# Performance work log

Measured on AMD Instinct MI355X. Metric: run time of the kernel, lower is better.

The kernel has to match this reference:

```python
import jax, jax.numpy as jnp
import numpy as np

BLOCK_SIZE = 128


def setup_inputs() -> dict:
    key = jax.random.key(0)
    kq, kk, kv = jax.random.split(key, 3)
    b, t, e = 16, 8192, 256
    Q = jax.random.normal(kq, (b, t, e), dtype=jnp.float32)
    K = jax.random.normal(kk, (b, t, e), dtype=jnp.float32)
    V = jax.random.normal(kv, (b, t, e), dtype=jnp.float32)
    return {"Q": Q, "K": K, "V": V}


def reference(Q, K, V):
    b, t, e = Q.shape
    bs = BLOCK_SIZE
    n = t // bs
    scale = 1.0 / jnp.sqrt(jnp.asarray(e, Q.dtype))
    Qb = Q.reshape(b, n, bs, e)
    Kb = K.reshape(b, n, bs, e)
    Vb = V.reshape(b, n, bs, e)
    # block-diagonal scores: [b, n, bs, bs]
    Z = jnp.einsum('bnqe,bnke->bnqk', Qb, Kb) * scale
    causal = jnp.triu(jnp.ones((bs, bs), dtype=bool), k=1)  # True above diagonal
    Z = jnp.where(causal, -jnp.inf, Z)
    A = jax.nn.softmax(Z, axis=-1)
    out = jnp.einsum('bnqk,bnke->bnqe', A, Vb).reshape(b, t, e)
    A_flat = A.reshape(b, t, bs)  # matches torch view(b, t, block_size)
    return out, A_flat
```

## Files before the change

kernel.cpp:

```cpp
#include <hip/hip_runtime.h>

#define T_  8192
#define E_  256
#define BS_ 128

typedef __attribute__((ext_vector_type(8))) short bf16x8;
typedef __attribute__((ext_vector_type(4))) float f32x4;

__device__ __forceinline__ unsigned short f2bf(float x) {
    unsigned int u = __float_as_uint(x);
    u += 0x7fffu + ((u >> 16) & 1u);
    return (unsigned short)(u >> 16);
}

__device__ __forceinline__ bf16x8 pack8(f32x4 a, f32x4 b) {
    bf16x8 r;
    r[0] = (short)f2bf(a[0]); r[1] = (short)f2bf(a[1]);
    r[2] = (short)f2bf(a[2]); r[3] = (short)f2bf(a[3]);
    r[4] = (short)f2bf(b[0]); r[5] = (short)f2bf(b[1]);
    r[6] = (short)f2bf(b[2]); r[7] = (short)f2bf(b[3]);
    return r;
}

__global__ __launch_bounds__(512, 4) void dba_fused(
        const float* __restrict__ Qg, const float* __restrict__ Kg,
        const float* __restrict__ Vg, float* __restrict__ Ag,
        float* __restrict__ Og)
{
    __shared__ unsigned short Sm[BS_ * E_];

    const int tid  = threadIdx.x;
    const int lane = tid & 63;
    const int w    = tid >> 6;
    const int cl   = lane & 15;
    const int g    = lane >> 4;
    const int bi   = blockIdx.x >> 6;
    const int ni   = blockIdx.x & 63;
    const int base  = (bi * T_ + ni * BS_) * E_;
    const int abase = (bi * T_ + ni * BS_) * BS_;

    {
        const int c4   = lane * 4;
        const int chnk = c4 >> 3;
        const int klow = c4 & 7;
        #pragma unroll 4
        for (int i = 0; i < 16; ++i) {
            const int n = i * 8 + w;
            f32x4 kv = __builtin_nontemporal_load((const f32x4*)(Kg + base + n * E_ + c4));
            const int cp = chnk ^ (n & 15);
            uint2 pk;
            pk.x = (unsigned)f2bf(kv[0]) | ((unsigned)f2bf(kv[1]) << 16);
            pk.y = (unsigned)f2bf(kv[2]) | ((unsigned)f2bf(kv[3]) << 16);
            *(uint2*)&Sm[n * E_ + cp * 8 + klow] = pk;
        }
    }
    __syncthreads();

    f32x4 acc[8];
    #pragma unroll
    for (int nt = 0; nt < 8; ++nt) acc[nt] = (f32x4){0.f, 0.f, 0.f, 0.f};

    const float* qp = Qg + base + (w * 16 + cl) * E_;
    f32x4 q0 = __builtin_nontemporal_load((const f32x4*)(qp + g * 8));
    f32x4 q1 = __builtin_nontemporal_load((const f32x4*)(qp + g * 8 + 4));

    for (int ks = 0; ks < 8; ++ks) {
        bf16x8 aq = pack8(q0, q1);
        if (ks < 7) {
            const int kn = (ks + 1) * 32 + g * 8;
            q0 = __builtin_nontemporal_load((const f32x4*)(qp + kn));
            q1 = __builtin_nontemporal_load((const f32x4*)(qp + kn + 4));
        }
        #pragma unroll
        for (int nt = 0; nt < 8; ++nt) {
            const int n  = nt * 16 + cl;
            const int cp = (ks * 4 + g) ^ cl;
            bf16x8 bk = *(const bf16x8*)&Sm[n * E_ + cp * 8];
            acc[nt] = __builtin_amdgcn_mfma_f32_16x16x32_bf16(aq, bk, acc[nt], 0, 0, 0);
        }
    }

    const float scale = 0.0625f;
    const float L2E   = 1.4426950408889634f;
    #pragma unroll
    for (int r = 0; r < 4; ++r) {
        const int q = w * 16 + g * 4 + r;
        float m = -__builtin_inff();
        #pragma unroll
        for (int nt = 0; nt < 8; ++nt) {
            const int c = nt * 16 + cl;
            float z = acc[nt][r] * scale;
            z = (c > q) ? -__builtin_inff() : z;
            acc[nt][r] = z;
            m = fmaxf(m, z);
        }
        m = fmaxf(m, __shfl_xor(m, 1));
        m = fmaxf(m, __shfl_xor(m, 2));
        m = fmaxf(m, __shfl_xor(m, 4));
        m = fmaxf(m, __shfl_xor(m, 8));
        float s = 0.f;
        #pragma unroll
        for (int nt = 0; nt < 8; ++nt) {
            const float p = exp2f((acc[nt][r] - m) * L2E);
            acc[nt][r] = p;
            s += p;
        }
        s += __shfl_xor(s, 1);
        s += __shfl_xor(s, 2);
        s += __shfl_xor(s, 4);
        s += __shfl_xor(s, 8);
        const float rinv = __builtin_amdgcn_rcpf(s);
        #pragma unroll
        for (int nt = 0; nt < 8; ++nt)
            acc[nt][r] *= rinv;
    }

    #pragma unroll
    for (int nt = 0; nt < 8; ++nt)
        #pragma unroll
        for (int r = 0; r < 4; ++r)
            Ag[abase + (w * 16 + g * 4 + r) * BS_ + nt * 16 + cl] = acc[nt][r];

    __syncthreads();

    {
        const int n  = tid & 255;
        const int kh = (tid >> 8) * 64;
        const int nx = n & 15;
        #pragma unroll 4
        for (int i = 0; i < 16; ++i) {
            const int k = kh + i * 4;
            const float* vp = Vg + base + k * E_ + n;
            const float v0 = __builtin_nontemporal_load(vp);
            const float v1 = __builtin_nontemporal_load(vp + E_);
            const float v2 = __builtin_nontemporal_load(vp + 2 * E_);
            const float v3 = __builtin_nontemporal_load(vp + 3 * E_);
            const int cp = (k >> 3) ^ nx;
            uint2 pk;
            pk.x = (unsigned)f2bf(v0) | ((unsigned)f2bf(v1) << 16);
            pk.y = (unsigned)f2bf(v2) | ((unsigned)f2bf(v3) << 16);
            *(uint2*)&Sm[n * BS_ + cp * 8 + (k & 7)] = pk;
        }
    }
    __syncthreads();

    f32x4 acc2[16];
    #pragma unroll
    for (int nt = 0; nt < 16; ++nt) acc2[nt] = (f32x4){0.f, 0.f, 0.f, 0.f};

    const float* ap = Ag + abase + (w * 16 + cl) * BS_;
    f32x4 a0 = *(const f32x4*)(ap + g * 8);
    f32x4 a1 = *(const f32x4*)(ap + g * 8 + 4);

    for (int ks = 0; ks < 4; ++ks) {
        bf16x8 fa = pack8(a0, a1);
        if (ks < 3) {
            const int kn = (ks + 1) * 32 + g * 8;
            a0 = *(const f32x4*)(ap + kn);
            a1 = *(const f32x4*)(ap + kn + 4);
        }
        #pragma unroll
        for (int nt = 0; nt < 16; ++nt) {
            const int nn = nt * 16 + cl;
            const int cp = (ks * 4 + g) ^ cl;
            bf16x8 bv = *(const bf16x8*)&Sm[nn * BS_ + cp * 8];
            acc2[nt] = __builtin_amdgcn_mfma_f32_16x16x32_bf16(fa, bv, acc2[nt], 0, 0, 0);
        }
    }

    #pragma unroll
    for (int nt = 0; nt < 16; ++nt)
        #pragma unroll
        for (int r = 0; r < 4; ++r)
            __builtin_nontemporal_store(acc2[nt][r],
                Og + base + (w * 16 + g * 4 + r) * E_ + nt * 16 + cl);
}

extern "C" void kernel_launch(void* const* d_in, const int* in_sizes, int n_in,
                              void* d_out, int out_size, void* d_ws, size_t ws_size,
                              hipStream_t stream) {
    const float* Q = (const float*)d_in[0];
    const float* K = (const float*)d_in[1];
    const float* V = (const float*)d_in[2];
    float* O = (float*)d_out;
    const int b = in_sizes[0] / (T_ * E_);
    float* A = O + (size_t)b * T_ * E_;
    dim3 grid(b * (T_ / BS_));
    dim3 block(512);
    dba_fused<<<grid, block, 0, stream>>>(Q, K, V, A, O);
}
```

Measured before the change: 438.7 us.

## Stage P in LDS and stream V from registers for the PV matmul

The PV stage is restructured. The softmax probabilities are written as bf16 into shared memory instead of being read back from global A. Each wave now owns 32 output columns and takes V directly from global into registers as the MFMA B operand, with V loads issued early and double-buffered across k-steps. This removes the global round-trip of A, the V staging pass through LDS and one barrier, and overlaps V loads with softmax. In exchange it raises register pressure (vb and acc2 arrays), and the scalar V loads are strided column-wise, which may coalesce less well.

```diff
diff --git a/kernel.cpp b/kernel.cpp
--- a/kernel.cpp
+++ b/kernel.cpp
@@ -20,6 +20,11 @@
     r[4] = (short)f2bf(b[0]); r[5] = (short)f2bf(b[1]);
     r[6] = (short)f2bf(b[2]); r[7] = (short)f2bf(b[3]);
     return r;
+}
+
+__device__ __forceinline__ void lds_barrier() {
+    asm volatile("s_waitcnt lgkmcnt(0)" ::: "memory");
+    __builtin_amdgcn_s_barrier();
 }
 
 __global__ __launch_bounds__(512, 4) void dba_fused(
@@ -38,12 +43,17 @@
     const int ni   = blockIdx.x & 63;
     const int base  = (bi * T_ + ni * BS_) * E_;
     const int abase = (bi * T_ + ni * BS_) * BS_;
+    const int vcol  = w * 32 + cl;
+
+    const float* qp = Qg + base + (w * 16 + cl) * E_;
+    f32x4 q0 = __builtin_nontemporal_load((const f32x4*)(qp + g * 8));
+    f32x4 q1 = __builtin_nontemporal_load((const f32x4*)(qp + g * 8 + 4));
 
     {
         const int c4   = lane * 4;
         const int chnk = c4 >> 3;
         const int klow = c4 & 7;
-        #pragma unroll 4
+        #pragma unroll 8
         for (int i = 0; i < 16; ++i) {
             const int n = i * 8 + w;
             f32x4 kv = __builtin_nontemporal_load((const f32x4*)(Kg + base + n * E_ + c4));
@@ -54,15 +64,11 @@
             *(uint2*)&Sm[n * E_ + cp * 8 + klow] = pk;
         }
     }
-    __syncthreads();
+    lds_barrier();
 
     f32x4 acc[8];
     #pragma unroll
     for (int nt = 0; nt < 8; ++nt) acc[nt] = (f32x4){0.f, 0.f, 0.f, 0.f};
-
-    const float* qp = Qg + base + (w * 16 + cl) * E_;
-    f32x4 q0 = __builtin_nontemporal_load((const f32x4*)(qp + g * 8));
-    f32x4 q1 = __builtin_nontemporal_load((const f32x4*)(qp + g * 8 + 4));
 
     for (int ks = 0; ks < 8; ++ks) {
         bf16x8 aq = pack8(q0, q1);
@@ -80,6 +86,16 @@
         }
     }
 
+    float vb[2][16];
+    #pragma unroll
+    for (int t = 0; t < 16; ++t)
+        vb[0][t] = __builtin_nontemporal_load(
+            Vg + base + (g * 8 + (t & 7)) * E_ + vcol + (t >> 3) * 16);
+    #pragma unroll
+    for (int t = 0; t < 16; ++t)
+        vb[1][t] = __builtin_nontemporal_load(
+            Vg + base + (32 + g * 8 + (t & 7)) * E_ + vcol + (t >> 3) * 16);
+
     const float scale = 0.0625f;
     const float L2E   = 1.4426950408889634f;
     #pragma unroll
@@ -119,61 +135,60 @@
     for (int nt = 0; nt < 8; ++nt)
         #pragma unroll
         for (int r = 0; r < 4; ++r)
-            Ag[abase + (w * 16 + g * 4 + r) * BS_ + nt * 16 + cl] = acc[nt][r];
-
-    __syncthreads();
-
-    {
-        const int n  = tid & 255;
-        const int kh = (tid >> 8) * 64;
-        const int nx = n & 15;
-        #pragma unroll 4
-        for (int i = 0; i < 16; ++i) {
-            const int k = kh + i * 4;
-            const float* vp = Vg + base + k * E_ + n;
-            const float v0 = __builtin_nontemporal_load(vp);
-            const float v1 = __builtin_nontemporal_load(vp + E_);
-            const float v2 = __builtin_nontemporal_load(vp + 2 * E_);
-            const float v3 = __builtin_nontemporal_load(vp + 3 * E_);
-            const int cp = (k >> 3) ^ nx;
-            uint2 pk;
-            pk.x = (unsigned)f2bf(v0) | ((unsigned)f2bf(v1) << 16);
-            pk.y = (unsigned)f2bf(v2) | ((unsigned)f2bf(v3) << 16);
-            *(uint2*)&Sm[n * BS_ + cp * 8 + (k & 7)] = pk;
-        }
-    }
-    __syncthreads();
-
-    f32x4 acc2[16];
-    #pragma unroll
-    for (int nt = 0; nt < 16; ++nt) acc2[nt] = (f32x4){0.f, 0.f, 0.f, 0.f};
-
-    const float* ap = Ag + abase + (w * 16 + cl) * BS_;
-    f32x4 a0 = *(const f32x4*)(ap + g * 8);
-    f32x4 a1 = *(const f32x4*)(ap + g * 8 + 4);
-
+            __builtin_nontemporal_store(acc[nt][r],
+                Ag + abase + (w * 16 + g * 4 + r) * BS_ + nt * 16 + cl);
+
+    lds_barrier();
+
+    #pragma unroll
+    for (int nt = 0; nt < 8; ++nt)
+        #pragma unroll
+        for (int r = 0; r < 4; ++r) {
+            const int q = w * 16 + g * 4 + r;
+            const int k = nt * 16 + cl;
+            Sm[q * BS_ + (((k >> 3) ^ (g * 4 + r)) * 8) + (k & 7)] = f2bf(acc[nt][r]);
+        }
+
+    lds_barrier();
+
+    f32x4 acc2[8][2];
+    #pragma unroll
+    for (int mt = 0; mt < 8; ++mt) {
+        acc2[mt][0] = (f32x4){0.f, 0.f, 0.f, 0.f};
+        acc2[mt][1] = (f32x4){0.f, 0.f, 0.f, 0.f};
+    }
+
+    #pragma unroll
     for (int ks = 0; ks < 4; ++ks) {
-        bf16x8 fa = pack8(a0, a1);
-        if (ks < 3) {
-            const int kn = (ks + 1) * 32 + g * 8;
-            a0 = *(const f32x4*)(ap + kn);
-            a1 = *(const f32x4*)(ap + kn + 4);
-        }
-        #pragma unroll
-        for (int nt = 0; nt < 16; ++nt) {
-            const int nn = nt * 16 + cl;
-            const int cp = (ks * 4 + g) ^ cl;
-            bf16x8 bv = *(const bf16x8*)&Sm[nn * BS_ + cp * 8];
-            acc2[nt] = __builtin_amdgcn_mfma_f32_16x16x32_bf16(fa, bv, acc2[nt], 0, 0, 0);
-        }
-    }
-
-    #pragma unroll
-    for (int nt = 0; nt < 16; ++nt)
-        #pragma unroll
-        for (int r = 0; r < 4; ++r)
-            __builtin_nontemporal_store(acc2[nt][r],
-                Og + base + (w * 16 + g * 4 + r) * E_ + nt * 16 + cl);
+        bf16x8 bv0, bv1;
+        #pragma unroll
+        for (int j = 0; j < 8; ++j) {
+            bv0[j] = (short)f2bf(vb[ks & 1][j]);
+            bv1[j] = (short)f2bf(vb[ks & 1][8 + j]);
+        }
+        if (ks < 2) {
+            #pragma unroll
+            for (int t = 0; t < 16; ++t)
+                vb[ks & 1][t] = __builtin_nontemporal_load(
+                    Vg + base + ((ks + 2) * 32 + g * 8 + (t & 7)) * E_ + vcol + (t >> 3) * 16);
+        }
+        #pragma unroll
+        for (int mt = 0; mt < 8; ++mt) {
+            const int q = mt * 16 + cl;
+            const bf16x8 pa = *(const bf16x8*)&Sm[q * BS_ + (((ks * 4 + g) ^ cl) * 8)];
+            acc2[mt][0] = __builtin_amdgcn_mfma_f32_16x16x32_bf16(pa, bv0, acc2[mt][0], 0, 0, 0);
+            acc2[mt][1] = __builtin_amdgcn_mfma_f32_16x16x32_bf16(pa, bv1, acc2[mt][1], 0, 0, 0);
+        }
+    }
+
+    #pragma unroll
+    for (int mt = 0; mt < 8; ++mt)
+        #pragma unroll
+        for (int n2 = 0; n2 < 2; ++n2)
+            #pragma unroll
+            for (int r = 0; r < 4; ++r)
+                __builtin_nontemporal_store(acc2[mt][n2][r],
+                    Og + base + (mt * 16 + g * 4 + r) * E_ + vcol + n2 * 16);
 }
 
 extern "C" void kernel_launch(void* const* d_in, const int* in_sizes, int n_in,
```

New measurement: 444.6 us. Within noise of the previous version (+1.3%).
